# Performance work log

Measured on AMD Instinct MI355X. Metric: run time of the kernel, lower is better.

## Reference

```python
import jax, jax.numpy as jnp
import numpy as np

H = 8          # n_heads
LORA_SCALE = 1.0


def _lora(x, down, up):
    # nn.Linear convention: y = x @ W.T ; down:[r,in], up:[out,r]
    return (x @ down.T) @ up.T


def setup_inputs() -> dict:
    key = jax.random.key(0)
    ks = jax.random.split(key, 16)
    B, S, D, R = 4, 2048, 640, 4
    std = 1.0 / np.sqrt(D)
    inp = {
        "hidden_states": jax.random.normal(ks[0], (B, S, D), jnp.float32),
        "wq": jax.random.normal(ks[1], (D, D), jnp.float32) * std,
        "wk": jax.random.normal(ks[2], (D, D), jnp.float32) * std,
        "wv": jax.random.normal(ks[3], (D, D), jnp.float32) * std,
        "wo": jax.random.normal(ks[4], (D, D), jnp.float32) * std,
        "bo": jax.random.normal(ks[5], (D,), jnp.float32) * 0.02,
        "q_down": jax.random.normal(ks[6], (R, D), jnp.float32) * (1.0 / R),
        "q_up": jax.random.normal(ks[7], (D, R), jnp.float32) * 0.02,
        "k_down": jax.random.normal(ks[8], (R, D), jnp.float32) * (1.0 / R),
        "k_up": jax.random.normal(ks[9], (D, R), jnp.float32) * 0.02,
        "v_down": jax.random.normal(ks[10], (R, D), jnp.float32) * (1.0 / R),
        "v_up": jax.random.normal(ks[11], (D, R), jnp.float32) * 0.02,
        "o_down": jax.random.normal(ks[12], (R, D), jnp.float32) * (1.0 / R),
        "o_up": jax.random.normal(ks[13], (D, R), jnp.float32) * 0.02,
    }
    return inp


def reference(hidden_states, wq, wk, wv, wo, bo,
              q_down, q_up, k_down, k_up, v_down, v_up, o_down, o_up):
    B, S, D = hidden_states.shape
    hd = D // H
    sm_scale = 1.0 / np.sqrt(hd)

    x = hidden_states  # self-attention: encoder_hidden_states = hidden_states
    q = x @ wq.T + LORA_SCALE * _lora(x, q_down, q_up)
    k = x @ wk.T + LORA_SCALE * _lora(x, k_down, k_up)
    v = x @ wv.T + LORA_SCALE * _lora(x, v_down, v_up)

    # head_to_batch_dim: [B,S,D] -> [B,H,S,hd]
    q = q.reshape(B, S, H, hd).transpose(0, 2, 1, 3)
    k = k.reshape(B, S, H, hd).transpose(0, 2, 1, 3)
    v = v.reshape(B, S, H, hd).transpose(0, 2, 1, 3)

    # get_attention_scores: baddbmm(beta=0, alpha=1/sqrt(hd)) + softmax
    scores = jnp.einsum("bhqd,bhkd->bhqk", q, k) * sm_scale
    probs = jax.nn.softmax(scores, axis=-1)
    attn_out = jnp.einsum("bhqk,bhkd->bhqd", probs, v)

    # batch_to_head_dim: [B,H,S,hd] -> [B,S,D]
    attn_out = attn_out.transpose(0, 2, 1, 3).reshape(B, S, D)

    # out projection (with bias) + LoRA on the pre-projection hidden states
    out = attn_out @ wo.T + bo + LORA_SCALE * _lora(attn_out, o_down, o_up)
    # to_out[1] is dropout -> identity at eval
    return out
```

## Files before the change

kernel.cpp:

```cpp
#include <hip/hip_runtime.h>

typedef unsigned short u16;
typedef unsigned int u32;
typedef unsigned long long u64;

typedef __bf16 bf16x8 __attribute__((ext_vector_type(8)));
typedef float f32x4 __attribute__((ext_vector_type(4)));
typedef float f32x16 __attribute__((ext_vector_type(16)));

__device__ __forceinline__ float b2f(u16 u) {
    union { u32 i; float f; } c; c.i = ((u32)u) << 16; return c.f;
}
__device__ __forceinline__ u16 f2b(float f) {
    union { float f; u32 i; } c; c.f = f;
    u32 r = c.i + 0x7fffu + ((c.i >> 16) & 1u);
    return (u16)(r >> 16);
}
__device__ __forceinline__ u32 cvt_pk_bf16(float a, float b) {
    u32 r;
    asm("v_cvt_pk_bf16_f32 %0, %1, %2" : "=v"(r) : "v"(a), "v"(b));
    return r;
}
__device__ __forceinline__ float fexp2(float x) {
    float r;
    asm("v_exp_f32 %0, %1" : "=v"(r) : "v"(x));
    return r;
}

__device__ __forceinline__ f32x4 mfma16(bf16x8 a, bf16x8 b, f32x4 c) {
    return __builtin_amdgcn_mfma_f32_16x16x32_bf16(a, b, c, 0, 0, 0);
}
__device__ __forceinline__ f32x16 mfma32(bf16x8 a, bf16x8 b, f32x16 c) {
    return __builtin_amdgcn_mfma_f32_32x32x16_bf16(a, b, c, 0, 0, 0);
}

__device__ __forceinline__ void lds_cp16(const u16* gsrc, u16* ldst) {
    __builtin_amdgcn_global_load_lds(
        (const __attribute__((address_space(1))) u32*)gsrc,
        (__attribute__((address_space(3))) u32*)ldst, 16, 0, 0);
}

struct ConvJobs {
    const float* s[4];
    u16* d[4];
};

__global__ __launch_bounds__(256) void convert_w(ConvJobs J) {
    int j = blockIdx.y;
    int i = blockIdx.x * 256 + threadIdx.x;
    float4 v = ((const float4*)J.s[j])[i];
    ushort4 o;
    o.x = f2b(v.x); o.y = f2b(v.y); o.z = f2b(v.z); o.w = f2b(v.w);
    ((ushort4*)J.d[j])[i] = o;
}

__global__ __launch_bounds__(256) void fuse_x(const float* __restrict__ x,
                                              const float* __restrict__ qd,
                                              const float* __restrict__ kd,
                                              const float* __restrict__ vd,
                                              u16* __restrict__ xb,
                                              float* __restrict__ T) {
    int m = blockIdx.x * 4 + (threadIdx.x >> 6);
    int lane = threadIdx.x & 63;
    const float* row = x + (size_t)m * 640;
    u16* orow = xb + (size_t)m * 640;
    float acc[12];
#pragma unroll
    for (int r = 0; r < 12; ++r) acc[r] = 0.f;
#pragma unroll
    for (int ii = 0; ii < 10; ++ii) {
        int i = lane + ii * 64;
        float a = row[i];
        orow[i] = f2b(a);
#pragma unroll
        for (int r = 0; r < 4; ++r) {
            acc[r]     += a * qd[r * 640 + i];
            acc[4 + r] += a * kd[r * 640 + i];
            acc[8 + r] += a * vd[r * 640 + i];
        }
    }
#pragma unroll
    for (int off = 32; off > 0; off >>= 1)
#pragma unroll
        for (int r = 0; r < 12; ++r) acc[r] += __shfl_xor(acc[r], off);
    if (lane == 0) {
#pragma unroll
        for (int p = 0; p < 3; ++p) {
            float4* t = (float4*)(T + ((size_t)p * 8192 + m) * 4);
            *t = make_float4(acc[p * 4], acc[p * 4 + 1], acc[p * 4 + 2], acc[p * 4 + 3]);
        }
    }
}

__global__ __launch_bounds__(256) void lora_down_o(const u16* __restrict__ A,
                                                   const float* __restrict__ dn,
                                                   float* __restrict__ T) {
    int m = blockIdx.x * 4 + (threadIdx.x >> 6);
    int lane = threadIdx.x & 63;
    const u16* arow = A + (size_t)m * 640;
    float a0 = 0.f, a1 = 0.f, a2 = 0.f, a3 = 0.f;
    for (int i = lane; i < 640; i += 64) {
        float a = b2f(arow[i]);
        a0 += a * dn[i];
        a1 += a * dn[640 + i];
        a2 += a * dn[1280 + i];
        a3 += a * dn[1920 + i];
    }
#pragma unroll
    for (int off = 32; off > 0; off >>= 1) {
        a0 += __shfl_xor(a0, off);
        a1 += __shfl_xor(a1, off);
        a2 += __shfl_xor(a2, off);
        a3 += __shfl_xor(a3, off);
    }
    if (lane == 0) {
        float4* t = (float4*)(T + (size_t)m * 4);
        *t = make_float4(a0, a1, a2, a3);
    }
}

struct QkvPtrs {
    const u16* W[3];
    const float* up[3];
    void* out[3];
    float scale[3];
};

__global__ __launch_bounds__(256) void gemm_bt(const u16* __restrict__ A, QkvPtrs P,
                                               const float* __restrict__ T,
                                               const float* __restrict__ bias, int mode) {
    int z = blockIdx.z;
    const u16* W = P.W[z];
    const float* up = P.up[z];
    const float scl = P.scale[z];
    const float* Tz = T + (size_t)z * 8192 * 4;
    int m0 = blockIdx.x * 128, n0 = blockIdx.y * 128;
    int tid = threadIdx.x, lane = tid & 63, wid = tid >> 6;
    int g = lane >> 4, l15 = lane & 15;
    __shared__ __align__(16) u16 As[3][4096];
    __shared__ __align__(16) u16 Bs[3][4096];
    f32x4 acc[4][4] = {};
    int wm = (wid & 1) * 64, wn = (wid >> 1) * 64;

    int r0 = tid >> 2, cb = (tid & 3) * 8;
    const u16* pA = A + (size_t)(m0 + r0) * 640 + cb;
    const u16* pB = W + (size_t)(n0 + r0) * 640 + cb;

    auto stage = [&](int buf, int k0) {
        u16* da = &As[buf][tid * 8];
        u16* db = &Bs[buf][tid * 8];
        lds_cp16(pA + k0, da);
        lds_cp16(pA + 40960 + k0, da + 2048);
        lds_cp16(pB + k0, db);
        lds_cp16(pB + 40960 + k0, db + 2048);
    };
    auto compute = [&](int cur) {
        const u16* as = &As[cur][0];
        const u16* bs = &Bs[cur][0];
        bf16x8 af[4], bfv[4];
#pragma unroll
        for (int q4 = 0; q4 < 4; ++q4) {
            af[q4]  = *(const bf16x8*)(as + (wm + q4 * 16 + l15) * 32 + g * 8);
            bfv[q4] = *(const bf16x8*)(bs + (wn + q4 * 16 + l15) * 32 + g * 8);
        }
#pragma unroll
        for (int i = 0; i < 4; ++i)
#pragma unroll
            for (int j = 0; j < 4; ++j)
                acc[i][j] = mfma16(af[i], bfv[j], acc[i][j]);
    };

    stage(0, 0);
    stage(1, 32);
    int cur = 0;
    for (int t = 0; t < 19; ++t) {
        asm volatile("s_waitcnt vmcnt(4)" ::: "memory");
        __builtin_amdgcn_s_barrier();
        asm volatile("" ::: "memory");
        if (t < 18) stage((cur == 0) ? 2 : cur - 1, (t + 2) * 32);
        compute(cur);
        cur = (cur == 2) ? 0 : cur + 1;
    }
    asm volatile("s_waitcnt vmcnt(0)" ::: "memory");
    __builtin_amdgcn_s_barrier();
    asm volatile("" ::: "memory");
    compute(cur);

    float4 upv[4];
    float bv[4];
#pragma unroll
    for (int j = 0; j < 4; ++j) {
        int n = n0 + wn + j * 16 + l15;
        upv[j] = *(const float4*)(up + n * 4);
        bv[j] = mode ? bias[n] : 0.f;
    }
    float* outf = (float*)P.out[z];
    u16* outb = (u16*)P.out[z];
#pragma unroll
    for (int i = 0; i < 4; ++i) {
#pragma unroll
        for (int r = 0; r < 4; ++r) {
            int m = m0 + wm + i * 16 + g * 4 + r;
            const float4 tv = *(const float4*)(Tz + (size_t)m * 4);
#pragma unroll
            for (int j = 0; j < 4; ++j) {
                int n = n0 + wn + j * 16 + l15;
                float v = acc[i][j][r] + tv.x * upv[j].x + tv.y * upv[j].y +
                          tv.z * upv[j].z + tv.w * upv[j].w + bv[j];
                if (mode) {
                    outf[(size_t)m * 640 + n] = v;
                } else {
                    int bb = m >> 11, s = m & 2047;
                    int h = n / 80, d = n - h * 80;
                    outb[(((size_t)bb * 8 + h) * 2048 + s) * 80 + d] = f2b(v * scl);
                }
            }
        }
    }
}

__global__ __launch_bounds__(256) void transpose_v(const u16* __restrict__ Vin,
                                                   u16* __restrict__ Vout) {
    __shared__ u32 lds32[64 * 41];
    int bh = blockIdx.y;
    int s0 = blockIdx.x * 64;
    int tid = threadIdx.x;
    const u16* in = Vin + (size_t)bh * 2048 * 80;
    u16* out = Vout + (size_t)bh * 96 * 2048;

    for (int t = tid; t < 640; t += 256) {
        int s = t / 10, c = t - s * 10;
        uint4 v = *(const uint4*)(in + (size_t)(s0 + s) * 80 + c * 8);
        u32* p = lds32 + s * 41 + c * 4;
        p[0] = v.x; p[1] = v.y; p[2] = v.z; p[3] = v.w;
    }
    __syncthreads();
    for (int t = tid; t < 640; t += 256) {
        int d = t >> 3, c8 = t & 7;
        int dp = d >> 1, hi = d & 1;
        u16 vals[8];
#pragma unroll
        for (int j = 0; j < 8; ++j) {
            u32 w = lds32[(c8 * 8 + j) * 41 + dp];
            vals[j] = hi ? (u16)(w >> 16) : (u16)(w & 0xffff);
        }
        u16* dst = out + (size_t)d * 2048 + s0 + (c8 >> 1) * 16 + (c8 & 1) * 4;
        *(uint2*)dst = *(const uint2*)(vals);
        *(uint2*)(dst + 8) = *(const uint2*)(vals + 4);
    }
    for (int t = tid; t < 1024; t += 256) {
        int r = t >> 6, c = t & 63;
        out[(size_t)(80 + r) * 2048 + s0 + c] = (r == 0) ? 0x3F80 : 0;
    }
}

__global__ __launch_bounds__(512) void flash_attn(const u16* __restrict__ Q,
                                                  const u16* __restrict__ K,
                                                  const u16* __restrict__ Vt_g,
                                                  u16* __restrict__ O) {
    int bh = blockIdx.y;
    int q0 = blockIdx.x * 256;
    int tid = threadIdx.x;
    int lane = tid & 63, wid = tid >> 6, l31 = lane & 31, h2 = lane >> 5;
    const size_t base = (size_t)bh * 2048 * 80;
    const size_t vbase = (size_t)bh * 96 * 2048;

    __shared__ __align__(16) u16 lds[2 * 5632 + 2 * 7200];
    u16* Ks0 = lds;
    u16* Vt0 = lds + 11264;

    bf16x8 qf[5];
    {
        int qrow = q0 + wid * 32 + l31;
#pragma unroll
        for (int ks = 0; ks < 5; ++ks)
            qf[ks] = *(const bf16x8*)(Q + base + (size_t)qrow * 80 + ks * 16 + h2 * 8);
    }

    f32x16 oa[3] = {};
    const float C2 = 17.312340490667562f;

    auto stage = [&](int buf, int kt) {
#pragma unroll
        for (int it = 0; it < 4; ++it) {
            int c = tid + it * 512;
            if (c < 704) {
                int row = c / 11, col = c - row * 11;
                lds_cp16(K + base + (size_t)(kt + row) * 80 + col * 8,
                         Ks0 + buf * 5632 + c * 8);
            } else if (c < 1600) {
                int t = c - 704;
                int row = t / 9, col = t - row * 9;
                lds_cp16(Vt_g + vbase + (size_t)row * 2048 + kt + col * 8,
                         Vt0 + buf * 7200 + t * 8);
            }
        }
    };

    stage(0, 0);
    __syncthreads();

    for (int i = 0; i < 32; ++i) {
        int cur = i & 1;
        if (i < 31) stage(cur ^ 1, (i + 1) * 64);

        const u16* ks = Ks0 + cur * 5632;
        const u16* vt = Vt0 + cur * 7200;

#pragma unroll
        for (int kk2 = 0; kk2 < 2; ++kk2) {
            f32x16 s = {};
            __builtin_amdgcn_s_setprio(1);
#pragma unroll
            for (int ks5 = 0; ks5 < 5; ++ks5) {
                bf16x8 kf = *(const bf16x8*)(ks + (kk2 * 32 + l31) * 88 + ks5 * 16 + h2 * 8);
                s = mfma32(kf, qf[ks5], s);
            }
            __builtin_amdgcn_s_setprio(0);
            u32 d[8];
#pragma unroll
            for (int j = 0; j < 8; ++j)
                d[j] = cvt_pk_bf16(fexp2(s[2 * j] - C2), fexp2(s[2 * j + 1] - C2));
            __builtin_amdgcn_s_setprio(1);
#pragma unroll
            for (int sl = 0; sl < 2; ++sl) {
                union { u32 w[4]; bf16x8 v; } pa;
                pa.w[0] = d[4 * sl + 0];
                pa.w[1] = d[4 * sl + 1];
                pa.w[2] = d[4 * sl + 2];
                pa.w[3] = d[4 * sl + 3];
#pragma unroll
                for (int nt = 0; nt < 3; ++nt) {
                    bf16x8 vf = *(const bf16x8*)(vt + (nt * 32 + l31) * 72 +
                                                 kk2 * 32 + sl * 16 + h2 * 8);
                    oa[nt] = mfma32(pa.v, vf, oa[nt]);
                }
            }
            __builtin_amdgcn_s_setprio(0);
        }
        __syncthreads();
    }

    int b = bh >> 3, h = bh & 7;
    float inv[16];
#pragma unroll
    for (int reg = 0; reg < 16; ++reg)
        inv[reg] = 1.f / __shfl(oa[2][reg], (lane & 32) + 16, 64);
#pragma unroll
    for (int nt = 0; nt < 3; ++nt) {
        int vd = nt * 32 + l31;
        if (vd < 80) {
#pragma unroll
            for (int reg = 0; reg < 16; ++reg) {
                int q = q0 + wid * 32 + (reg & 3) + 8 * (reg >> 2) + 4 * h2;
                O[((size_t)(b * 2048 + q)) * 640 + h * 80 + vd] = f2b(oa[nt][reg] * inv[reg]);
            }
        }
    }
}

extern "C" void kernel_launch(void* const* d_in, const int* in_sizes, int n_in,
                              void* d_out, int out_size, void* d_ws, size_t ws_size,
                              hipStream_t stream) {
    const float* x      = (const float*)d_in[0];
    const float* wq     = (const float*)d_in[1];
    const float* wk     = (const float*)d_in[2];
    const float* wv     = (const float*)d_in[3];
    const float* wo     = (const float*)d_in[4];
    const float* bo     = (const float*)d_in[5];
    const float* q_down = (const float*)d_in[6];
    const float* q_up   = (const float*)d_in[7];
    const float* k_down = (const float*)d_in[8];
    const float* k_up   = (const float*)d_in[9];
    const float* v_down = (const float*)d_in[10];
    const float* v_up   = (const float*)d_in[11];
    const float* o_down = (const float*)d_in[12];
    const float* o_up   = (const float*)d_in[13];

    char* ws = (char*)d_ws;
    u16* xb    = (u16*)(ws);
    u16* vT_ws = (u16*)(ws);
    u16* wbv   = (u16*)(ws + 10485760);
    u16* wbq   = (u16*)(ws + 11304960);
    u16* wbk   = (u16*)(ws + 12124160);
    u16* wbo   = (u16*)(ws + 12943360);
    u16* q_ws  = (u16*)(ws + 13762560);
    u16* k_ws  = (u16*)(ws + 24248320);
    u16* v_ws  = (u16*)(ws + 34734080);
    u16* attn  = (u16*)(ws + 45219840);
    float* Tq  = (float*)(ws + 55705600);
    float* To  = (float*)(ws + 56098816);

    ConvJobs cj;
    cj.s[0] = wq; cj.d[0] = wbq;
    cj.s[1] = wk; cj.d[1] = wbk;
    cj.s[2] = wv; cj.d[2] = wbv;
    cj.s[3] = wo; cj.d[3] = wbo;
    convert_w<<<dim3(400, 4), 256, 0, stream>>>(cj);

    fuse_x<<<2048, 256, 0, stream>>>(x, q_down, k_down, v_down, xb, Tq);

    QkvPtrs pq;
    pq.W[0] = wbq; pq.W[1] = wbk; pq.W[2] = wbv;
    pq.up[0] = q_up; pq.up[1] = k_up; pq.up[2] = v_up;
    pq.out[0] = q_ws; pq.out[1] = k_ws; pq.out[2] = v_ws;
    pq.scale[0] = 0.11180339887498949f * 1.4426950408889634f;
    pq.scale[1] = 1.0f;
    pq.scale[2] = 1.0f;
    gemm_bt<<<dim3(64, 5, 3), 256, 0, stream>>>(xb, pq, Tq, bo, 0);

    transpose_v<<<dim3(32, 32), 256, 0, stream>>>(v_ws, vT_ws);

    flash_attn<<<dim3(8, 32), 512, 0, stream>>>(q_ws, k_ws, vT_ws, attn);

    lora_down_o<<<2048, 256, 0, stream>>>(attn, o_down, To);

    QkvPtrs po;
    po.W[0] = wbo; po.W[1] = wbo; po.W[2] = wbo;
    po.up[0] = o_up; po.up[1] = o_up; po.up[2] = o_up;
    po.out[0] = d_out; po.out[1] = d_out; po.out[2] = d_out;
    po.scale[0] = 1.0f; po.scale[1] = 1.0f; po.scale[2] = 1.0f;
    gemm_bt<<<dim3(64, 5, 1), 256, 0, stream>>>(attn, po, To, bo, 1);
}
```

Baseline: 239.4 us.

## Write transposed V directly from QKV GEMM epilogue and merge prep kernels

```diff
diff --git a/kernel.cpp b/kernel.cpp
--- a/kernel.cpp
+++ b/kernel.cpp
@@ -16,6 +16,9 @@
     u32 r = c.i + 0x7fffu + ((c.i >> 16) & 1u);
     return (u16)(r >> 16);
 }
+__device__ __forceinline__ u32 pack2(float a, float b) {
+    return (u32)f2b(a) | ((u32)f2b(b) << 16);
+}
 __device__ __forceinline__ u32 cvt_pk_bf16(float a, float b) {
     u32 r;
     asm("v_cvt_pk_bf16_f32 %0, %1, %2" : "=v"(r) : "v"(a), "v"(b));
@@ -45,50 +48,63 @@
     u16* d[4];
 };
 
-__global__ __launch_bounds__(256) void convert_w(ConvJobs J) {
-    int j = blockIdx.y;
-    int i = blockIdx.x * 256 + threadIdx.x;
-    float4 v = ((const float4*)J.s[j])[i];
-    ushort4 o;
-    o.x = f2b(v.x); o.y = f2b(v.y); o.z = f2b(v.z); o.w = f2b(v.w);
-    ((ushort4*)J.d[j])[i] = o;
-}
-
-__global__ __launch_bounds__(256) void fuse_x(const float* __restrict__ x,
-                                              const float* __restrict__ qd,
-                                              const float* __restrict__ kd,
-                                              const float* __restrict__ vd,
-                                              u16* __restrict__ xb,
-                                              float* __restrict__ T) {
-    int m = blockIdx.x * 4 + (threadIdx.x >> 6);
-    int lane = threadIdx.x & 63;
-    const float* row = x + (size_t)m * 640;
-    u16* orow = xb + (size_t)m * 640;
-    float acc[12];
-#pragma unroll
-    for (int r = 0; r < 12; ++r) acc[r] = 0.f;
-#pragma unroll
-    for (int ii = 0; ii < 10; ++ii) {
-        int i = lane + ii * 64;
-        float a = row[i];
-        orow[i] = f2b(a);
-#pragma unroll
-        for (int r = 0; r < 4; ++r) {
-            acc[r]     += a * qd[r * 640 + i];
-            acc[4 + r] += a * kd[r * 640 + i];
-            acc[8 + r] += a * vd[r * 640 + i];
-        }
-    }
-#pragma unroll
-    for (int off = 32; off > 0; off >>= 1)
-#pragma unroll
-        for (int r = 0; r < 12; ++r) acc[r] += __shfl_xor(acc[r], off);
-    if (lane == 0) {
-#pragma unroll
-        for (int p = 0; p < 3; ++p) {
-            float4* t = (float4*)(T + ((size_t)p * 8192 + m) * 4);
-            *t = make_float4(acc[p * 4], acc[p * 4 + 1], acc[p * 4 + 2], acc[p * 4 + 3]);
-        }
+__global__ __launch_bounds__(256) void prep(ConvJobs J,
+                                            const float* __restrict__ x,
+                                            const float* __restrict__ qd,
+                                            const float* __restrict__ kd,
+                                            const float* __restrict__ vd,
+                                            u16* __restrict__ xb,
+                                            float* __restrict__ T,
+                                            u16* __restrict__ vt, int do_pad) {
+    int bx = blockIdx.x;
+    if (bx < 1600) {
+        int j = bx / 400;
+        int i = (bx - j * 400) * 256 + threadIdx.x;
+        float4 v = ((const float4*)J.s[j])[i];
+        ushort4 o;
+        o.x = f2b(v.x); o.y = f2b(v.y); o.z = f2b(v.z); o.w = f2b(v.w);
+        ((ushort4*)J.d[j])[i] = o;
+    } else if (bx < 3648) {
+        int m = (bx - 1600) * 4 + (threadIdx.x >> 6);
+        int lane = threadIdx.x & 63;
+        const float* row = x + (size_t)m * 640;
+        u16* orow = xb + (size_t)m * 640;
+        float acc[12];
+#pragma unroll
+        for (int r = 0; r < 12; ++r) acc[r] = 0.f;
+#pragma unroll
+        for (int ii = 0; ii < 10; ++ii) {
+            int i = lane + ii * 64;
+            float a = row[i];
+            orow[i] = f2b(a);
+#pragma unroll
+            for (int r = 0; r < 4; ++r) {
+                acc[r]     += a * qd[r * 640 + i];
+                acc[4 + r] += a * kd[r * 640 + i];
+                acc[8 + r] += a * vd[r * 640 + i];
+            }
+        }
+#pragma unroll
+        for (int off = 32; off > 0; off >>= 1)
+#pragma unroll
+            for (int r = 0; r < 12; ++r) acc[r] += __shfl_xor(acc[r], off);
+        if (lane == 0) {
+#pragma unroll
+            for (int p = 0; p < 3; ++p) {
+                float4* t = (float4*)(T + ((size_t)p * 8192 + m) * 4);
+                *t = make_float4(acc[p * 4], acc[p * 4 + 1], acc[p * 4 + 2],
+                                 acc[p * 4 + 3]);
+            }
+        }
+    } else if (do_pad) {
+        int idx = (bx - 3648) * 256 + threadIdx.x;
+        int q = idx * 4;
+        int bh = q >> 15;
+        int rem = q & 32767;
+        int row = rem >> 11, col = rem & 2047;
+        u16 val = (row == 0) ? (u16)0x3F80 : (u16)0;
+        ushort4 o = make_ushort4(val, val, val, val);
+        *(ushort4*)(vt + ((size_t)bh * 96 + 80 + row) * 2048 + col) = o;
     }
 }
 
@@ -124,21 +140,24 @@
     const float* up[3];
     void* out[3];
     float scale[3];
+    int mode[3];
 };
 
 __global__ __launch_bounds__(256) void gemm_bt(const u16* __restrict__ A, QkvPtrs P,
                                                const float* __restrict__ T,
-                                               const float* __restrict__ bias, int mode) {
+                                               const float* __restrict__ bias) {
     int z = blockIdx.z;
     const u16* W = P.W[z];
     const float* up = P.up[z];
     const float scl = P.scale[z];
+    const int md = P.mode[z];
     const float* Tz = T + (size_t)z * 8192 * 4;
     int m0 = blockIdx.x * 128, n0 = blockIdx.y * 128;
     int tid = threadIdx.x, lane = tid & 63, wid = tid >> 6;
     int g = lane >> 4, l15 = lane & 15;
-    __shared__ __align__(16) u16 As[3][4096];
-    __shared__ __align__(16) u16 Bs[3][4096];
+    __shared__ __align__(16) u16 smem[24576];
+    u16* As_ = smem;
+    u16* Bs_ = smem + 12288;
     f32x4 acc[4][4] = {};
     int wm = (wid & 1) * 64, wn = (wid >> 1) * 64;
 
@@ -147,16 +166,16 @@
     const u16* pB = W + (size_t)(n0 + r0) * 640 + cb;
 
     auto stage = [&](int buf, int k0) {
-        u16* da = &As[buf][tid * 8];
-        u16* db = &Bs[buf][tid * 8];
+        u16* da = As_ + buf * 4096 + tid * 8;
+        u16* db = Bs_ + buf * 4096 + tid * 8;
         lds_cp16(pA + k0, da);
         lds_cp16(pA + 40960 + k0, da + 2048);
         lds_cp16(pB + k0, db);
         lds_cp16(pB + 40960 + k0, db + 2048);
     };
     auto compute = [&](int cur) {
-        const u16* as = &As[cur][0];
-        const u16* bs = &Bs[cur][0];
+        const u16* as = As_ + cur * 4096;
+        const u16* bs = Bs_ + cur * 4096;
         bf16x8 af[4], bfv[4];
 #pragma unroll
         for (int q4 = 0; q4 < 4; ++q4) {
@@ -192,8 +211,48 @@
     for (int j = 0; j < 4; ++j) {
         int n = n0 + wn + j * 16 + l15;
         upv[j] = *(const float4*)(up + n * 4);
-        bv[j] = mode ? bias[n] : 0.f;
-    }
+        bv[j] = (md == 1) ? bias[n] : 0.f;
+    }
+
+    if (md == 2) {
+        __syncthreads();
+        u16* Tl = smem;
+#pragma unroll
+        for (int i = 0; i < 4; ++i) {
+#pragma unroll
+            for (int j = 0; j < 4; ++j) {
+                float vs[4];
+#pragma unroll
+                for (int r = 0; r < 4; ++r) {
+                    int m = m0 + wm + i * 16 + g * 4 + r;
+                    const float4 tv = *(const float4*)(Tz + (size_t)m * 4);
+                    vs[r] = acc[i][j][r] + tv.x * upv[j].x + tv.y * upv[j].y +
+                            tv.z * upv[j].z + tv.w * upv[j].w;
+                }
+                uint2 pk;
+                pk.x = pack2(vs[0], vs[1]);
+                pk.y = pack2(vs[2], vs[3]);
+                *(uint2*)(Tl + (wn + j * 16 + l15) * 136 + wm + i * 16 + g * 4) = pk;
+            }
+        }
+        __syncthreads();
+        int bb2 = m0 >> 11;
+        int sl0 = m0 & 2047;
+        u16* outb_ = (u16*)P.out[z];
+#pragma unroll
+        for (int it = 0; it < 16; ++it) {
+            int qq = it * 256 + tid;
+            int row = qq >> 5;
+            int pos = (qq & 31) * 4;
+            int ss = (pos & ~12) | ((pos & 4) << 1) | ((pos & 8) >> 1);
+            uint2 val = *(const uint2*)(Tl + row * 136 + ss);
+            int n = n0 + row;
+            int h = n / 80, d = n - h * 80;
+            *(uint2*)(outb_ + (((size_t)bb2 * 8 + h) * 96 + d) * 2048 + sl0 + pos) = val;
+        }
+        return;
+    }
+
     float* outf = (float*)P.out[z];
     u16* outb = (u16*)P.out[z];
 #pragma unroll
@@ -207,7 +266,7 @@
                 int n = n0 + wn + j * 16 + l15;
                 float v = acc[i][j][r] + tv.x * upv[j].x + tv.y * upv[j].y +
                           tv.z * upv[j].z + tv.w * upv[j].w + bv[j];
-                if (mode) {
+                if (md == 1) {
                     outf[(size_t)m * 640 + n] = v;
                 } else {
                     int bb = m >> 11, s = m & 2047;
@@ -379,7 +438,6 @@
 
     char* ws = (char*)d_ws;
     u16* xb    = (u16*)(ws);
-    u16* vT_ws = (u16*)(ws);
     u16* wbv   = (u16*)(ws + 10485760);
     u16* wbq   = (u16*)(ws + 11304960);
     u16* wbk   = (u16*)(ws + 12124160);
@@ -391,25 +449,33 @@
     float* Tq  = (float*)(ws + 55705600);
     float* To  = (float*)(ws + 56098816);
 
+    const size_t vt_off = 56360960;
+    const size_t vt_need = vt_off + 12582912 + 16384;
+    const bool direct_vt = (ws_size >= vt_need);
+    u16* vT_ws = direct_vt ? (u16*)(ws + vt_off)
+                           : (u16*)(ws);
+
     ConvJobs cj;
     cj.s[0] = wq; cj.d[0] = wbq;
     cj.s[1] = wk; cj.d[1] = wbk;
     cj.s[2] = wv; cj.d[2] = wbv;
     cj.s[3] = wo; cj.d[3] = wbo;
-    convert_w<<<dim3(400, 4), 256, 0, stream>>>(cj);
-
-    fuse_x<<<2048, 256, 0, stream>>>(x, q_down, k_down, v_down, xb, Tq);
+    prep<<<4672, 256, 0, stream>>>(cj, x, q_down, k_down, v_down, xb, Tq,
+                                   vT_ws, direct_vt ? 1 : 0);
 
     QkvPtrs pq;
     pq.W[0] = wbq; pq.W[1] = wbk; pq.W[2] = wbv;
     pq.up[0] = q_up; pq.up[1] = k_up; pq.up[2] = v_up;
-    pq.out[0] = q_ws; pq.out[1] = k_ws; pq.out[2] = v_ws;
+    pq.out[0] = q_ws; pq.out[1] = k_ws;
+    pq.out[2] = direct_vt ? (void*)vT_ws : (void*)v_ws;
     pq.scale[0] = 0.11180339887498949f * 1.4426950408889634f;
     pq.scale[1] = 1.0f;
     pq.scale[2] = 1.0f;
-    gemm_bt<<<dim3(64, 5, 3), 256, 0, stream>>>(xb, pq, Tq, bo, 0);
-
-    transpose_v<<<dim3(32, 32), 256, 0, stream>>>(v_ws, vT_ws);
+    pq.mode[0] = 0; pq.mode[1] = 0; pq.mode[2] = direct_vt ? 2 : 0;
+    gemm_bt<<<dim3(64, 5, 3), 256, 0, stream>>>(xb, pq, Tq, bo);
+
+    if (!direct_vt)
+        transpose_v<<<dim3(32, 32), 256, 0, stream>>>(v_ws, vT_ws);
 
     flash_attn<<<dim3(8, 32), 512, 0, stream>>>(q_ws, k_ws, vT_ws, attn);
 
@@ -420,5 +486,6 @@
     po.up[0] = o_up; po.up[1] = o_up; po.up[2] = o_up;
     po.out[0] = d_out; po.out[1] = d_out; po.out[2] = d_out;
     po.scale[0] = 1.0f; po.scale[1] = 1.0f; po.scale[2] = 1.0f;
-    gemm_bt<<<dim3(64, 5, 1), 256, 0, stream>>>(attn, po, To, bo, 1);
-}
+    po.mode[0] = 1; po.mode[1] = 1; po.mode[2] = 1;
+    gemm_bt<<<dim3(64, 5, 1), 256, 0, stream>>>(attn, po, To, bo);
+}
```

After: 213.2 us. -10.9%, faster.
